# Optimization experiments

Measured on AMD Instinct MI355X. Metric: run time of the kernel, lower is better.

## Reference

```python
import jax, jax.numpy as jnp
import numpy as np

N = 8192  # number of proposals


def setup_inputs() -> dict:
    key = jax.random.key(0)
    k1, k2, k3 = jax.random.split(key, 3)
    xy = jax.random.uniform(k1, (N, 2), dtype=jnp.float32) * 1000.0   # top-left corners
    wh = jax.random.uniform(k2, (N, 2), dtype=jnp.float32) * 120.0 + 4.0  # widths/heights
    conf = jax.random.uniform(k3, (N, 1), dtype=jnp.float32)
    preds = jnp.concatenate([xy, xy + wh, conf], axis=1)  # [N,5] x1,y1,x2,y2,conf
    return {"preds": preds, "thresh": 0.5, "max_proposals": 1000}


def _nms_keep_mask(boxes_sorted, thresh):
    # boxes_sorted: [N,4] sorted by descending confidence
    x1, y1, x2, y2 = (boxes_sorted[:, i] for i in range(4))
    area = (x2 - x1) * (y2 - y1)                               # [N]
    ix1 = jnp.maximum(x1[:, None], x1[None, :])
    iy1 = jnp.maximum(y1[:, None], y1[None, :])
    ix2 = jnp.minimum(x2[:, None], x2[None, :])
    iy2 = jnp.minimum(y2[:, None], y2[None, :])
    iw = jnp.maximum(ix2 - ix1, 0.0)
    ih = jnp.maximum(iy2 - iy1, 0.0)
    inter = iw * ih                                            # [N,N]
    iou = inter / (area[:, None] + area[None, :] - inter + 1e-12)
    n = boxes_sorted.shape[0]
    later = jnp.arange(n)[None, :] > jnp.arange(n)[:, None]    # strictly lower-priority boxes

    def body(i, keep):
        # if box i survives, suppress all later boxes overlapping it above thresh
        sup = keep[i] & later[i] & (iou[i] > thresh)
        return keep & ~sup

    return jax.lax.fori_loop(0, n, body, jnp.ones((n,), dtype=bool))


def reference(preds, thresh, max_proposals):
    # thresh < 0 -> identity (original early return); implemented with thresh >= 0 path
    order = jnp.argsort(-preds[:, 4])          # descending confidence
    boxes_sorted = preds[order, :4]
    keep = _nms_keep_mask(boxes_sorted, thresh)  # [N] bool, in sorted order
    n = preds.shape[0]
    # stable pack: kept positions first (ascending = descending confidence), pad at end
    rank = jnp.where(keep, jnp.arange(n), n)
    pos = jnp.argsort(rank)[:max_proposals]     # [M] positions in sorted order
    valid = keep[pos]                           # [M] which slots are real
    keep_idx = jnp.where(valid, order[pos], -1)  # indices into original preds, -1 pad
    kept = preds[jnp.clip(keep_idx, 0)]          # [M,5]
    kept = jnp.where(valid[:, None], kept, 0.0)
    return kept, keep_idx
```

## Files before the change

### kernel.cpp

```cpp
#include <hip/hip_runtime.h>

typedef unsigned long long u64;

#define FSLOTS 16
#define RCUT 2048

__global__ __launch_bounds__(256)
void k_rank_part(const float* __restrict__ preds, int n, int cpb,
                 int* __restrict__ pc) {
  __shared__ float cs[1024];
  int c0 = blockIdx.y * cpb;
  int cn = min(cpb, n - c0);
  for (int j = threadIdx.x; j < cn; j += blockDim.x)
    cs[j] = preds[(c0 + j) * 5 + 4];
  __syncthreads();
  int i = blockIdx.x * blockDim.x + threadIdx.x;
  if (i >= n) return;
  float ci = preds[i * 5 + 4];
  int cnt = 0;
  const float4* cs4 = (const float4*)cs;
  int cn4 = cn >> 2;
  for (int j4 = 0; j4 < cn4; ++j4) {
    float4 c4 = cs4[j4];
    int jb = c0 + j4 * 4;
    cnt += (c4.x > ci) || (c4.x == ci && (jb + 0) < i);
    cnt += (c4.y > ci) || (c4.y == ci && (jb + 1) < i);
    cnt += (c4.z > ci) || (c4.z == ci && (jb + 2) < i);
    cnt += (c4.w > ci) || (c4.w == ci && (jb + 3) < i);
  }
  for (int j = cn4 * 4; j < cn; ++j)
    cnt += (cs[j] > ci) || (cs[j] == ci && (c0 + j) < i);
  pc[(size_t)blockIdx.y * n + i] = cnt;
}

__global__ __launch_bounds__(256)
void k_scatter(const float* __restrict__ preds, const int* __restrict__ pc,
               int n, int nyb, float* __restrict__ sboxes,
               int* __restrict__ sidx, int* __restrict__ rowcnt) {
  int i = blockIdx.x * blockDim.x + threadIdx.x;
  if (i >= n) return;
  rowcnt[i] = 0;
  int pos = 0;
  for (int y = 0; y < nyb; ++y) pos += pc[(size_t)y * n + i];
  sboxes[pos * 4 + 0] = preds[i * 5 + 0];
  sboxes[pos * 4 + 1] = preds[i * 5 + 1];
  sboxes[pos * 4 + 2] = preds[i * 5 + 2];
  sboxes[pos * 4 + 3] = preds[i * 5 + 3];
  sidx[pos] = i;
}

__global__ void k_mask(const float* __restrict__ sboxes, int n,
                       const float* __restrict__ thr_p,
                       u64* __restrict__ M, u64* __restrict__ D1,
                       int* __restrict__ rowcnt, int* __restrict__ rowlist,
                       int nw, int Rw, int mode, const int* __restrict__ done) {
  int wx, ry;
  if (mode == 0) {
    wx = blockIdx.x; ry = blockIdx.y;
    if (wx < ry) return;
  } else {
    if (*done) return;
    int u = blockIdx.x + (Rw * (Rw + 1)) / 2;
    int w = (int)((sqrt(8.0 * u + 1.0) - 1.0) * 0.5);
    while ((w + 1) * (w + 2) / 2 <= u) ++w;
    while (w * (w + 1) / 2 > u) --w;
    wx = w; ry = u - w * (w + 1) / 2;
  }
  int lane = threadIdx.x;

  __shared__ float4 cb[64];
  __shared__ float cbar[64];
  const float4* sb4 = (const float4*)sboxes;
  int col0 = wx * 64;
  int cj = col0 + lane;
  int cjc = cj < n ? cj : n - 1;
  {
    float4 b4 = sb4[cjc];
    cb[lane] = b4;
    cbar[lane] = __fmul_rn(__fsub_rn(b4.z, b4.x), __fsub_rn(b4.w, b4.y));
  }
  __syncthreads();

  int row = ry * 64 + lane;
  if (row >= n) return;
  float th = *thr_p;
  float4 r4 = sb4[row];
  float rarea = __fmul_rn(__fsub_rn(r4.z, r4.x), __fsub_rn(r4.w, r4.y));

  u64 w = 0;
#pragma unroll 8
  for (int j = 0; j < 64; ++j) {
    float4 c4 = cb[j];
    float ix1 = fmaxf(r4.x, c4.x);
    float iy1 = fmaxf(r4.y, c4.y);
    float ix2 = fminf(r4.z, c4.z);
    float iy2 = fminf(r4.w, c4.w);
    float iw = fmaxf(__fsub_rn(ix2, ix1), 0.0f);
    float ih = fmaxf(__fsub_rn(iy2, iy1), 0.0f);
    float inter = __fmul_rn(iw, ih);
    float denom = __fadd_rn(__fsub_rn(__fadd_rn(rarea, cbar[j]), inter), 1e-12f);
    float iou = __fdiv_rn(inter, denom);
    int col = col0 + j;
    bool sup = (col > row) && (col < n) && (iou > th);
    w |= ((u64)sup) << j;
  }
  M[(size_t)row * nw + wx] = w;
  if (wx == ry) D1[row] = w;
  int pcw = (int)__popcll(w);
  if (pcw) {
    int base = atomicAdd(&rowcnt[row], pcw);
    u64 w2 = w;
    int k = 0;
    while (w2) {
      int j = (int)__builtin_ctzll(w2);
      w2 &= w2 - 1;
      int idx = base + k;
      if (idx < FSLOTS) rowlist[(size_t)row * FSLOTS + idx] = col0 + j;
      ++k;
    }
  }
}

__device__ __forceinline__ u64 bcast64(u64 v, int b) {
  unsigned lo = __builtin_amdgcn_readlane((unsigned)v, b);
  unsigned hi = __builtin_amdgcn_readlane((unsigned)(v >> 32), b);
  return ((u64)hi << 32) | lo;
}

__device__ __forceinline__ u64 sgpr64(u64 v) {
  unsigned lo = __builtin_amdgcn_readfirstlane((unsigned)v);
  unsigned hi = __builtin_amdgcn_readfirstlane((unsigned)(v >> 32));
  return ((u64)hi << 32) | lo;
}

__device__ __forceinline__ u64 wor64(u64 v) {
#pragma unroll
  for (int off = 32; off; off >>= 1)
    v |= __shfl_xor(v, off, 64);
  return v;
}

#define APPLYJ(JV, T)                                                      \
  if ((T) < lim_) {                                                        \
    int j_ = (JV);                                                         \
    atomicAnd(&live[j_ >> 6], ~((u64)1 << (j_ & 63)));                     \
  }

#define CHUNK(c, BND, RC, LA, LB, LC, LD)                                  \
  if (out < maxp && (c) < nch) {                                           \
    u64 rem_ = sgpr64(live[(c)]);                                          \
    if (rem_) {                                                            \
      u64 K_;                                                              \
      u64 my_ = ((rem_ >> lane) & 1) ? (BND) : 0;                          \
      u64 A_ = sgpr64(wor64(my_));                                         \
      u64 hot_ = rem_ & A_;                                                \
      if (!hot_) {                                                         \
        K_ = rem_;                                                         \
      } else {                                                             \
        u64 defK_ = rem_ & ~A_;                                            \
        u64 myk_ = ((defK_ >> lane) & 1) ? (BND) : 0;                      \
        u64 S_ = sgpr64(wor64(myk_));                                      \
        K_ = defK_;                                                        \
        while (hot_) {                                                     \
          int b_ = __builtin_amdgcn_readfirstlane(                         \
              (int)__builtin_ctzll(hot_));                                 \
          hot_ &= hot_ - 1;                                                \
          if (!((S_ >> b_) & 1)) {                                         \
            K_ |= (u64)1 << b_;                                            \
            S_ |= bcast64(BND, b_);                                        \
          }                                                                \
        }                                                                  \
      }                                                                    \
      int kc_ = (int)__popcll(K_);                                         \
      bool mine_ = (K_ >> lane) & 1;                                       \
      if (mine_) {                                                         \
        int pos_ = out + (int)__popcll(K_ & (((u64)1 << lane) - 1));       \
        if (pos_ < maxp) sel[pos_] = (c) * 64 + lane;                      \
      }                                                                    \
      out += kc_;                                                          \
      if (kc_ > 0 && out < maxp) {                                         \
        int lim_ = mine_ ? ((RC) < FSLOTS ? (RC) : FSLOTS) : 0;            \
        APPLYJ((LA).x, 0)  APPLYJ((LA).y, 1)                               \
        APPLYJ((LA).z, 2)  APPLYJ((LA).w, 3)                               \
        APPLYJ((LB).x, 4)  APPLYJ((LB).y, 5)                               \
        APPLYJ((LB).z, 6)  APPLYJ((LB).w, 7)                               \
        APPLYJ((LC).x, 8)  APPLYJ((LC).y, 9)                               \
        APPLYJ((LC).z, 10) APPLYJ((LC).w, 11)                              \
        APPLYJ((LD).x, 12) APPLYJ((LD).y, 13)                              \
        APPLYJ((LD).z, 14) APPLYJ((LD).w, 15)                              \
        u64 ovf_ = __ballot(mine_ && (RC) > FSLOTS);                       \
        while (ovf_) {                                                     \
          int l_ = (int)__builtin_ctzll(ovf_);                             \
          ovf_ &= ovf_ - 1;                                                \
          int r_ = (c) * 64 + l_;                                          \
          u64 v0_ = (2 * lane < nch)                                       \
                        ? M[(size_t)r_ * nw + 2 * lane] : 0ULL;            \
          u64 v1_ = (2 * lane + 1 < nch)                                   \
                        ? M[(size_t)r_ * nw + 2 * lane + 1] : 0ULL;        \
          live[2 * lane] &= ~v0_;                                          \
          live[2 * lane + 1] &= ~v1_;                                      \
        }                                                                  \
      }                                                                    \
    }                                                                      \
    {                                                                      \
      int cc_ = (c) + 4;                                                   \
      if (cc_ < nch) {                                                     \
        int r_ = cc_ * 64 + lane;                                          \
        int rr_ = r_ < n ? r_ : n - 1;                                     \
        BND = D1[rr_];                                                     \
        RC = rowcnt[rr_];                                                  \
        const int4* lp_ = (const int4*)(rowlist + (size_t)rr_ * FSLOTS);   \
        LA = lp_[0]; LB = lp_[1]; LC = lp_[2]; LD = lp_[3];                \
      }                                                                    \
    }                                                                      \
  }

#define PREF(cc, BND, RC, LA, LB, LC, LD)                                  \
  if ((cc) < nch) {                                                        \
    int r_ = (cc) * 64 + lane;                                             \
    int rr_ = r_ < n ? r_ : n - 1;                                         \
    BND = D1[rr_];                                                         \
    RC = rowcnt[rr_];                                                      \
    const int4* lp_ = (const int4*)(rowlist + (size_t)rr_ * FSLOTS);       \
    LA = lp_[0]; LB = lp_[1]; LC = lp_[2]; LD = lp_[3];                    \
  }

#define SCAN_BODY(NCH_)                                                    \
  int nch = (NCH_);                                                        \
  for (int w = lane; w < 128; w += 64) {                                   \
    u64 m = 0;                                                             \
    if (w < nw) {                                                          \
      long long hi = (long long)(w + 1) * 64;                              \
      m = (hi <= n) ? ~0ULL                                                \
                    : ((n > (long long)w * 64)                             \
                           ? (((u64)1 << (n - w * 64)) - 1) : 0ULL);       \
    }                                                                      \
    live[w] = m;                                                           \
  }                                                                        \
  u64 b0 = 0, b1 = 0, b2 = 0, b3 = 0;                                      \
  int rc0 = 0, rc1 = 0, rc2 = 0, rc3 = 0;                                  \
  int4 l00 = {0,0,0,0}, l01 = {0,0,0,0}, l02 = {0,0,0,0}, l03 = {0,0,0,0}; \
  int4 l10 = {0,0,0,0}, l11 = {0,0,0,0}, l12 = {0,0,0,0}, l13 = {0,0,0,0}; \
  int4 l20 = {0,0,0,0}, l21 = {0,0,0,0}, l22 = {0,0,0,0}, l23 = {0,0,0,0}; \
  int4 l30 = {0,0,0,0}, l31 = {0,0,0,0}, l32 = {0,0,0,0}, l33 = {0,0,0,0}; \
  PREF(0, b0, rc0, l00, l01, l02, l03)                                     \
  PREF(1, b1, rc1, l10, l11, l12, l13)                                     \
  PREF(2, b2, rc2, l20, l21, l22, l23)                                     \
  PREF(3, b3, rc3, l30, l31, l32, l33)                                     \
  int out = 0;                                                             \
  for (int kk = 0; kk < nch && out < maxp; kk += 4) {                      \
    CHUNK(kk + 0, b0, rc0, l00, l01, l02, l03)                             \
    CHUNK(kk + 1, b1, rc1, l10, l11, l12, l13)                             \
    CHUNK(kk + 2, b2, rc2, l20, l21, l22, l23)                             \
    CHUNK(kk + 3, b3, rc3, l30, l31, l32, l33)                             \
  }

__global__ __launch_bounds__(64, 1)
void k_scan_try(const u64* __restrict__ M, const u64* __restrict__ D1,
                const int* __restrict__ rowcnt, const int* __restrict__ rowlist,
                int n, int nw, int maxp, int nch_lim,
                int* __restrict__ done,
                int* __restrict__ sel, int* __restrict__ cnt) {
  __shared__ u64 live[128];
  int lane = threadIdx.x;
  SCAN_BODY(nch_lim)
  if (lane == 0) {
    *cnt = (out < maxp) ? out : maxp;
    *done = (out >= maxp || nch_lim >= nw) ? 1 : 0;
  }
}

__global__ __launch_bounds__(256, 1)
void k_finish(const u64* __restrict__ M, const u64* __restrict__ D1,
              const int* __restrict__ rowcnt, const int* __restrict__ rowlist,
              const float* __restrict__ preds, const int* __restrict__ sidx,
              int n, int nw, int maxp, const int* __restrict__ done,
              int* __restrict__ sel, int* __restrict__ cnt,
              float* __restrict__ outp) {
  __shared__ u64 live[128];
  __shared__ int nk_s;
  int t = threadIdx.x;
  int dn = *done;
  if (!dn) {
    if (t < 64) {
      int lane = t;
      SCAN_BODY(nw)
      if (lane == 0) {
        int nk = (out < maxp) ? out : maxp;
        *cnt = nk;
        nk_s = nk;
      }
    }
  } else {
    if (t == 0) nk_s = *cnt;
  }
  __syncthreads();
  int nk = nk_s;
  for (int k = t; k < maxp; k += 256) {
    if (k < nk) {
      int p = sel[k];
      int orig = sidx[p];
#pragma unroll
      for (int q = 0; q < 5; ++q) outp[k * 5 + q] = preds[orig * 5 + q];
      outp[(size_t)maxp * 5 + k] = (float)orig;
    } else {
#pragma unroll
      for (int q = 0; q < 5; ++q) outp[k * 5 + q] = 0.0f;
      outp[(size_t)maxp * 5 + k] = -1.0f;
    }
  }
}

extern "C" void kernel_launch(void* const* d_in, const int* in_sizes, int n_in,
                              void* d_out, int out_size, void* d_ws, size_t ws_size,
                              hipStream_t stream) {
  const float* preds = (const float*)d_in[0];
  const float* thr   = (const float*)d_in[1];
  float* out = (float*)d_out;
  int n    = in_sizes[0] / 5;
  int maxp = out_size / 6;
  int nw   = (n + 63) / 64;
  int Rw   = (RCUT / 64 < nw) ? RCUT / 64 : nw;
  int cpb  = 1024;
  int nyb  = (n + cpb - 1) / cpb;
  int hiT  = (nw * (nw + 1)) / 2 - (Rw * (Rw + 1)) / 2;

  char* ws = (char*)d_ws;
  u64* M = (u64*)ws;
  size_t off = (size_t)n * nw * sizeof(u64);
  u64* D1 = (u64*)(ws + off);  off += (size_t)n * sizeof(u64);
  float* sboxes = (float*)(ws + off);  off += (size_t)n * 4 * sizeof(float);
  int*   sidx   = (int*)(ws + off);    off += (size_t)n * sizeof(int);
  int*   sel    = (int*)(ws + off);    off += (size_t)maxp * sizeof(int);
  int*   cnt    = (int*)(ws + off);    off += sizeof(int) * 4;
  int*   done   = (int*)(ws + off);    off += sizeof(int) * 4;
  int*   rowcnt = (int*)(ws + off);    off += (size_t)n * sizeof(int);
  int*   rowlist= (int*)(ws + off);    off += (size_t)n * FSLOTS * sizeof(int);
  int*   pc     = (int*)(ws + off);

  hipLaunchKernelGGL(k_rank_part, dim3((n + 255) / 256, nyb), dim3(256), 0,
                     stream, preds, n, cpb, pc);
  hipLaunchKernelGGL(k_scatter, dim3((n + 255) / 256), dim3(256), 0, stream,
                     preds, pc, n, nyb, sboxes, sidx, rowcnt);
  hipLaunchKernelGGL(k_mask, dim3(Rw, Rw), dim3(64), 0, stream,
                     sboxes, n, thr, M, D1, rowcnt, rowlist, nw, Rw, 0, done);
  hipLaunchKernelGGL(k_scan_try, dim3(1), dim3(64), 0, stream,
                     M, D1, rowcnt, rowlist, n, nw, maxp, Rw, done, sel, cnt);
  if (hiT > 0)
    hipLaunchKernelGGL(k_mask, dim3(hiT), dim3(64), 0, stream,
                       sboxes, n, thr, M, D1, rowcnt, rowlist, nw, Rw, 1, done);
  hipLaunchKernelGGL(k_finish, dim3(1), dim3(256), 0, stream,
                     M, D1, rowcnt, rowlist, preds, sidx, n, nw, maxp, done,
                     sel, cnt, out);
}
```

Before: 74.49 us.

## Fuse all NMS stages into one cooperative persistent kernel with grid syncs

Merges the six separate launches (rank, scatter, two mask passes, trial scan, finish) into a single cooperative kernel of 256 blocks that separates the phases with grid-wide barriers. Mask tiles are now handed out per wave through a grid-stride walk over the triangular tile index, and the finish phase runs across the whole grid instead of one block. The goal is to remove per-launch and inter-kernel gap overhead. In exchange it pays for six grid syncs, leaves most of the grid idle during the single-wave scan phases, and hardcodes the rank phase to 32x8 blocks (n=8192).

After: 215.7 us. 190% more time.

```diff
diff --git a/kernel.cpp b/kernel.cpp
--- a/kernel.cpp
+++ b/kernel.cpp
@@ -1,142 +1,26 @@
 #include <hip/hip_runtime.h>
+#include <hip/hip_cooperative_groups.h>
+
+namespace cg = cooperative_groups;
 
 typedef unsigned long long u64;
 
 #define FSLOTS 16
 #define RCUT 2048
-
-__global__ __launch_bounds__(256)
-void k_rank_part(const float* __restrict__ preds, int n, int cpb,
-                 int* __restrict__ pc) {
-  __shared__ float cs[1024];
-  int c0 = blockIdx.y * cpb;
-  int cn = min(cpb, n - c0);
-  for (int j = threadIdx.x; j < cn; j += blockDim.x)
-    cs[j] = preds[(c0 + j) * 5 + 4];
-  __syncthreads();
-  int i = blockIdx.x * blockDim.x + threadIdx.x;
-  if (i >= n) return;
-  float ci = preds[i * 5 + 4];
-  int cnt = 0;
-  const float4* cs4 = (const float4*)cs;
-  int cn4 = cn >> 2;
-  for (int j4 = 0; j4 < cn4; ++j4) {
-    float4 c4 = cs4[j4];
-    int jb = c0 + j4 * 4;
-    cnt += (c4.x > ci) || (c4.x == ci && (jb + 0) < i);
-    cnt += (c4.y > ci) || (c4.y == ci && (jb + 1) < i);
-    cnt += (c4.z > ci) || (c4.z == ci && (jb + 2) < i);
-    cnt += (c4.w > ci) || (c4.w == ci && (jb + 3) < i);
-  }
-  for (int j = cn4 * 4; j < cn; ++j)
-    cnt += (cs[j] > ci) || (cs[j] == ci && (c0 + j) < i);
-  pc[(size_t)blockIdx.y * n + i] = cnt;
-}
-
-__global__ __launch_bounds__(256)
-void k_scatter(const float* __restrict__ preds, const int* __restrict__ pc,
-               int n, int nyb, float* __restrict__ sboxes,
-               int* __restrict__ sidx, int* __restrict__ rowcnt) {
-  int i = blockIdx.x * blockDim.x + threadIdx.x;
-  if (i >= n) return;
-  rowcnt[i] = 0;
-  int pos = 0;
-  for (int y = 0; y < nyb; ++y) pos += pc[(size_t)y * n + i];
-  sboxes[pos * 4 + 0] = preds[i * 5 + 0];
-  sboxes[pos * 4 + 1] = preds[i * 5 + 1];
-  sboxes[pos * 4 + 2] = preds[i * 5 + 2];
-  sboxes[pos * 4 + 3] = preds[i * 5 + 3];
-  sidx[pos] = i;
-}
-
-__global__ void k_mask(const float* __restrict__ sboxes, int n,
-                       const float* __restrict__ thr_p,
-                       u64* __restrict__ M, u64* __restrict__ D1,
-                       int* __restrict__ rowcnt, int* __restrict__ rowlist,
-                       int nw, int Rw, int mode, const int* __restrict__ done) {
-  int wx, ry;
-  if (mode == 0) {
-    wx = blockIdx.x; ry = blockIdx.y;
-    if (wx < ry) return;
-  } else {
-    if (*done) return;
-    int u = blockIdx.x + (Rw * (Rw + 1)) / 2;
-    int w = (int)((sqrt(8.0 * u + 1.0) - 1.0) * 0.5);
-    while ((w + 1) * (w + 2) / 2 <= u) ++w;
-    while (w * (w + 1) / 2 > u) --w;
-    wx = w; ry = u - w * (w + 1) / 2;
-  }
-  int lane = threadIdx.x;
-
-  __shared__ float4 cb[64];
-  __shared__ float cbar[64];
-  const float4* sb4 = (const float4*)sboxes;
-  int col0 = wx * 64;
-  int cj = col0 + lane;
-  int cjc = cj < n ? cj : n - 1;
-  {
-    float4 b4 = sb4[cjc];
-    cb[lane] = b4;
-    cbar[lane] = __fmul_rn(__fsub_rn(b4.z, b4.x), __fsub_rn(b4.w, b4.y));
-  }
-  __syncthreads();
-
-  int row = ry * 64 + lane;
-  if (row >= n) return;
-  float th = *thr_p;
-  float4 r4 = sb4[row];
-  float rarea = __fmul_rn(__fsub_rn(r4.z, r4.x), __fsub_rn(r4.w, r4.y));
-
-  u64 w = 0;
-#pragma unroll 8
-  for (int j = 0; j < 64; ++j) {
-    float4 c4 = cb[j];
-    float ix1 = fmaxf(r4.x, c4.x);
-    float iy1 = fmaxf(r4.y, c4.y);
-    float ix2 = fminf(r4.z, c4.z);
-    float iy2 = fminf(r4.w, c4.w);
-    float iw = fmaxf(__fsub_rn(ix2, ix1), 0.0f);
-    float ih = fmaxf(__fsub_rn(iy2, iy1), 0.0f);
-    float inter = __fmul_rn(iw, ih);
-    float denom = __fadd_rn(__fsub_rn(__fadd_rn(rarea, cbar[j]), inter), 1e-12f);
-    float iou = __fdiv_rn(inter, denom);
-    int col = col0 + j;
-    bool sup = (col > row) && (col < n) && (iou > th);
-    w |= ((u64)sup) << j;
-  }
-  M[(size_t)row * nw + wx] = w;
-  if (wx == ry) D1[row] = w;
-  int pcw = (int)__popcll(w);
-  if (pcw) {
-    int base = atomicAdd(&rowcnt[row], pcw);
-    u64 w2 = w;
-    int k = 0;
-    while (w2) {
-      int j = (int)__builtin_ctzll(w2);
-      w2 &= w2 - 1;
-      int idx = base + k;
-      if (idx < FSLOTS) rowlist[(size_t)row * FSLOTS + idx] = col0 + j;
-      ++k;
-    }
-  }
-}
 
 __device__ __forceinline__ u64 bcast64(u64 v, int b) {
   unsigned lo = __builtin_amdgcn_readlane((unsigned)v, b);
   unsigned hi = __builtin_amdgcn_readlane((unsigned)(v >> 32), b);
   return ((u64)hi << 32) | lo;
 }
-
 __device__ __forceinline__ u64 sgpr64(u64 v) {
   unsigned lo = __builtin_amdgcn_readfirstlane((unsigned)v);
   unsigned hi = __builtin_amdgcn_readfirstlane((unsigned)(v >> 32));
   return ((u64)hi << 32) | lo;
 }
-
 __device__ __forceinline__ u64 wor64(u64 v) {
 #pragma unroll
-  for (int off = 32; off; off >>= 1)
-    v |= __shfl_xor(v, off, 64);
+  for (int off = 32; off; off >>= 1) v |= __shfl_xor(v, off, 64);
   return v;
 }
 
@@ -255,58 +139,189 @@
     CHUNK(kk + 3, b3, rc3, l30, l31, l32, l33)                             \
   }
 
-__global__ __launch_bounds__(64, 1)
-void k_scan_try(const u64* __restrict__ M, const u64* __restrict__ D1,
-                const int* __restrict__ rowcnt, const int* __restrict__ rowlist,
-                int n, int nw, int maxp, int nch_lim,
-                int* __restrict__ done,
-                int* __restrict__ sel, int* __restrict__ cnt) {
+__device__ __forceinline__ void do_tile(int wx, int ry, int lane,
+                                        const float4* sb4, float4* cb,
+                                        float* cbar, int n, float th,
+                                        u64* M, u64* D1, int* rowcnt,
+                                        int* rowlist, int nw) {
+  int col0 = wx * 64;
+  int cj = col0 + lane;
+  int cjc = cj < n ? cj : n - 1;
+  {
+    float4 b4 = sb4[cjc];
+    cb[lane] = b4;
+    cbar[lane] = __fmul_rn(__fsub_rn(b4.z, b4.x), __fsub_rn(b4.w, b4.y));
+  }
+  int row = ry * 64 + lane;
+  if (row >= n) return;
+  float4 r4 = sb4[row];
+  float rarea = __fmul_rn(__fsub_rn(r4.z, r4.x), __fsub_rn(r4.w, r4.y));
+  u64 w = 0;
+#pragma unroll 8
+  for (int j = 0; j < 64; ++j) {
+    float4 c4 = cb[j];
+    float ix1 = fmaxf(r4.x, c4.x);
+    float iy1 = fmaxf(r4.y, c4.y);
+    float ix2 = fminf(r4.z, c4.z);
+    float iy2 = fminf(r4.w, c4.w);
+    float iw = fmaxf(__fsub_rn(ix2, ix1), 0.0f);
+    float ih = fmaxf(__fsub_rn(iy2, iy1), 0.0f);
+    float inter = __fmul_rn(iw, ih);
+    float denom = __fadd_rn(__fsub_rn(__fadd_rn(rarea, cbar[j]), inter), 1e-12f);
+    float iou = __fdiv_rn(inter, denom);
+    int col = col0 + j;
+    bool sup = (col > row) && (col < n) && (iou > th);
+    w |= ((u64)sup) << j;
+  }
+  M[(size_t)row * nw + wx] = w;
+  if (wx == ry) D1[row] = w;
+  int pcw = (int)__popcll(w);
+  if (pcw) {
+    int base = atomicAdd(&rowcnt[row], pcw);
+    u64 w2 = w;
+    int k = 0;
+    while (w2) {
+      int j = (int)__builtin_ctzll(w2);
+      w2 &= w2 - 1;
+      int idx = base + k;
+      if (idx < FSLOTS) rowlist[(size_t)row * FSLOTS + idx] = col0 + j;
+      ++k;
+    }
+  }
+}
+
+__device__ __forceinline__ void tri_decode(int u, int* wxo, int* ryo) {
+  int w = (int)((sqrtf(8.0f * u + 1.0f) - 1.0f) * 0.5f);
+  while ((w + 1) * (w + 2) / 2 <= u) ++w;
+  while (w * (w + 1) / 2 > u) --w;
+  *wxo = w;
+  *ryo = u - w * (w + 1) / 2;
+}
+
+__global__ __launch_bounds__(256, 1)
+void k_nms(const float* __restrict__ preds, const float* __restrict__ thr_p,
+           u64* __restrict__ M, u64* __restrict__ D1,
+           int* __restrict__ rowcnt, int* __restrict__ rowlist,
+           int* __restrict__ pc, float* __restrict__ sboxes,
+           int* __restrict__ sidx, int* __restrict__ sel,
+           int* __restrict__ cnt, int* __restrict__ done,
+           int n, int nw, int maxp, int Rw,
+           float* __restrict__ outp) {
+  cg::grid_group grid = cg::this_grid();
+  int bid = blockIdx.x;
+  int t = threadIdx.x;
+  int wid = t >> 6, lane = t & 63;
+  int nblk = gridDim.x;
+  int nwav = nblk * 4;
+
+  __shared__ float cs[1024];
+  __shared__ float4 cbw[4][64];
+  __shared__ float cbarw[4][64];
   __shared__ u64 live[128];
-  int lane = threadIdx.x;
-  SCAN_BODY(nch_lim)
-  if (lane == 0) {
-    *cnt = (out < maxp) ? out : maxp;
-    *done = (out >= maxp || nch_lim >= nw) ? 1 : 0;
-  }
-}
-
-__global__ __launch_bounds__(256, 1)
-void k_finish(const u64* __restrict__ M, const u64* __restrict__ D1,
-              const int* __restrict__ rowcnt, const int* __restrict__ rowlist,
-              const float* __restrict__ preds, const int* __restrict__ sidx,
-              int n, int nw, int maxp, const int* __restrict__ done,
-              int* __restrict__ sel, int* __restrict__ cnt,
-              float* __restrict__ outp) {
-  __shared__ u64 live[128];
-  __shared__ int nk_s;
-  int t = threadIdx.x;
-  int dn = *done;
+
+  const float4* sb4 = (const float4*)sboxes;
+  float th = *thr_p;
+
+  {
+    int xb = bid & 31, yb = bid >> 5;
+    int c0 = yb * 1024;
+    int cn = n - c0; if (cn > 1024) cn = 1024;
+    if (cn > 0)
+      for (int j = t; j < cn; j += 256) cs[j] = preds[(c0 + j) * 5 + 4];
+    __syncthreads();
+    int i = xb * 256 + t;
+    if (i < n) {
+      int cn_ = cn > 0 ? cn : 0;
+      float ci = preds[i * 5 + 4];
+      int cntv = 0;
+      const float4* cs4 = (const float4*)cs;
+      int cn4 = cn_ >> 2;
+      for (int j4 = 0; j4 < cn4; ++j4) {
+        float4 c4 = cs4[j4];
+        int jb = c0 + j4 * 4;
+        cntv += (c4.x > ci) || (c4.x == ci && (jb + 0) < i);
+        cntv += (c4.y > ci) || (c4.y == ci && (jb + 1) < i);
+        cntv += (c4.z > ci) || (c4.z == ci && (jb + 2) < i);
+        cntv += (c4.w > ci) || (c4.w == ci && (jb + 3) < i);
+      }
+      for (int j = cn4 * 4; j < cn_; ++j)
+        cntv += (cs[j] > ci) || (cs[j] == ci && (c0 + j) < i);
+      pc[(size_t)yb * n + i] = cntv;
+    }
+  }
+  grid.sync();
+
+  for (int i = bid * 256 + t; i < n; i += nblk * 256) {
+    rowcnt[i] = 0;
+    int pos = 0;
+#pragma unroll
+    for (int y = 0; y < 8; ++y) pos += pc[(size_t)y * n + i];
+    sboxes[pos * 4 + 0] = preds[i * 5 + 0];
+    sboxes[pos * 4 + 1] = preds[i * 5 + 1];
+    sboxes[pos * 4 + 2] = preds[i * 5 + 2];
+    sboxes[pos * 4 + 3] = preds[i * 5 + 3];
+    sidx[pos] = i;
+  }
+  grid.sync();
+
+  {
+    int loTri = (Rw * (Rw + 1)) / 2;
+    for (int u = bid * 4 + wid; u < loTri; u += nwav) {
+      int wx, ry;
+      tri_decode(u, &wx, &ry);
+      do_tile(wx, ry, lane, sb4, cbw[wid], cbarw[wid], n, th,
+              M, D1, rowcnt, rowlist, nw);
+    }
+  }
+  grid.sync();
+
+  if (bid == 0 && t < 64) {
+    SCAN_BODY(Rw)
+    if (lane == 0) {
+      *cnt = (out < maxp) ? out : maxp;
+      *done = (out >= maxp || Rw >= nw) ? 1 : 0;
+      __threadfence();
+    }
+  }
+  grid.sync();
+
+  int dn = *(volatile int*)done;
+
   if (!dn) {
-    if (t < 64) {
-      int lane = t;
-      SCAN_BODY(nw)
-      if (lane == 0) {
-        int nk = (out < maxp) ? out : maxp;
-        *cnt = nk;
-        nk_s = nk;
+    int loTri = (Rw * (Rw + 1)) / 2;
+    int totTri = (nw * (nw + 1)) / 2;
+    for (int u = loTri + bid * 4 + wid; u < totTri; u += nwav) {
+      int wx, ry;
+      tri_decode(u, &wx, &ry);
+      do_tile(wx, ry, lane, sb4, cbw[wid], cbarw[wid], n, th,
+              M, D1, rowcnt, rowlist, nw);
+    }
+  }
+  grid.sync();
+
+  if (!dn && bid == 0 && t < 64) {
+    SCAN_BODY(nw)
+    if (lane == 0) {
+      *cnt = (out < maxp) ? out : maxp;
+      __threadfence();
+    }
+  }
+  grid.sync();
+
+  {
+    int nk = *(volatile int*)cnt;
+    for (int k = bid * 256 + t; k < maxp; k += nblk * 256) {
+      if (k < nk) {
+        int p = sel[k];
+        int orig = sidx[p];
+#pragma unroll
+        for (int q = 0; q < 5; ++q) outp[k * 5 + q] = preds[orig * 5 + q];
+        outp[(size_t)maxp * 5 + k] = (float)orig;
+      } else {
+#pragma unroll
+        for (int q = 0; q < 5; ++q) outp[k * 5 + q] = 0.0f;
+        outp[(size_t)maxp * 5 + k] = -1.0f;
       }
-    }
-  } else {
-    if (t == 0) nk_s = *cnt;
-  }
-  __syncthreads();
-  int nk = nk_s;
-  for (int k = t; k < maxp; k += 256) {
-    if (k < nk) {
-      int p = sel[k];
-      int orig = sidx[p];
-#pragma unroll
-      for (int q = 0; q < 5; ++q) outp[k * 5 + q] = preds[orig * 5 + q];
-      outp[(size_t)maxp * 5 + k] = (float)orig;
-    } else {
-#pragma unroll
-      for (int q = 0; q < 5; ++q) outp[k * 5 + q] = 0.0f;
-      outp[(size_t)maxp * 5 + k] = -1.0f;
     }
   }
 }
@@ -321,9 +336,6 @@
   int maxp = out_size / 6;
   int nw   = (n + 63) / 64;
   int Rw   = (RCUT / 64 < nw) ? RCUT / 64 : nw;
-  int cpb  = 1024;
-  int nyb  = (n + cpb - 1) / cpb;
-  int hiT  = (nw * (nw + 1)) / 2 - (Rw * (Rw + 1)) / 2;
 
   char* ws = (char*)d_ws;
   u64* M = (u64*)ws;
@@ -338,18 +350,8 @@
   int*   rowlist= (int*)(ws + off);    off += (size_t)n * FSLOTS * sizeof(int);
   int*   pc     = (int*)(ws + off);
 
-  hipLaunchKernelGGL(k_rank_part, dim3((n + 255) / 256, nyb), dim3(256), 0,
-                     stream, preds, n, cpb, pc);
-  hipLaunchKernelGGL(k_scatter, dim3((n + 255) / 256), dim3(256), 0, stream,
-                     preds, pc, n, nyb, sboxes, sidx, rowcnt);
-  hipLaunchKernelGGL(k_mask, dim3(Rw, Rw), dim3(64), 0, stream,
-                     sboxes, n, thr, M, D1, rowcnt, rowlist, nw, Rw, 0, done);
-  hipLaunchKernelGGL(k_scan_try, dim3(1), dim3(64), 0, stream,
-                     M, D1, rowcnt, rowlist, n, nw, maxp, Rw, done, sel, cnt);
-  if (hiT > 0)
-    hipLaunchKernelGGL(k_mask, dim3(hiT), dim3(64), 0, stream,
-                       sboxes, n, thr, M, D1, rowcnt, rowlist, nw, Rw, 1, done);
-  hipLaunchKernelGGL(k_finish, dim3(1), dim3(256), 0, stream,
-                     M, D1, rowcnt, rowlist, preds, sidx, n, nw, maxp, done,
-                     sel, cnt, out);
-}
+  void* args[] = {&preds, &thr, &M, &D1, &rowcnt, &rowlist, &pc, &sboxes,
+                  &sidx, &sel, &cnt, &done, &n, &nw, &maxp, &Rw, &out};
+  hipLaunchCooperativeKernel((void*)k_nms, dim3(256), dim3(256), args, 0,
+                             stream);
+}
```
